# Kernel optimization log

Measured on AMD Instinct MI355X. Metric: run time of the kernel, lower is better.

The kernel has to match this reference:

```python
import jax, jax.numpy as jnp
import numpy as np

H, N_EMB, D_EMB, D_UP = 1024, 8192, 512, 2048
B, T, BB, M, K_LABELS = 4, 4096, 512, 4096, 64


def _rms(x, w, eps=1e-6):
    xf = x.astype(jnp.float32)
    var = jnp.mean(xf * xf, axis=-1, keepdims=True)
    return (w * (xf * jax.lax.rsqrt(var + eps))).astype(x.dtype)


def setup_inputs() -> dict:
    key = jax.random.key(0)
    ks = jax.random.split(key, 8)
    bt = B * T
    inp = jax.random.normal(ks[0], (B, T, H), jnp.float32)
    w_k = jax.random.normal(ks[1], (N_EMB, H), jnp.float32) * 0.02
    w_v = jax.random.normal(ks[2], (N_EMB, D_EMB), jnp.float32) * 0.02
    w_up = jax.random.normal(ks[3], (D_UP, D_EMB), jnp.float32) * 0.02
    w_mix = jax.random.normal(ks[4], (H, D_UP + H), jnp.float32) * 0.02
    fw = jax.random.permutation(ks[5], bt)
    bw = jnp.argsort(fw)  # inverse permutation
    seq_sort = jax.random.randint(ks[6], (bt,), 0, K_LABELS)
    keep_cols = jnp.arange(M)  # keep first M of N_EMB rows
    emb_alloc = jnp.arange(N_EMB) % K_LABELS  # every label present among kept rows
    starts = jnp.zeros((bt,), jnp.int32)
    ends = jnp.full((bt,), M, jnp.int32)
    return {
        'input': inp, 'fw': fw, 'bw': bw, 'seq_sort': seq_sort,
        'keep_cols': keep_cols, 'emb_alloc': emb_alloc,
        'starts': starts, 'ends': ends, 'bb': BB,
        'w_k_weight': w_k, 'w_v_weight': w_v, 'w_up_weight': w_up,
        'w_mix_weight': w_mix,
        'norm_in_weight': jnp.ones((H,), jnp.float32),
        'norm_out_weight': jnp.ones((D_UP,), jnp.float32),
    }


def reference(input, fw, bw, seq_sort, keep_cols, emb_alloc, starts, ends, bb,
              w_k_weight, w_v_weight, w_up_weight, w_mix_weight,
              norm_in_weight, norm_out_weight):
    b, t, h = input.shape
    A = _rms(input, norm_in_weight)                      # [b,t,h]
    Bm = w_k_weight[keep_cols]                           # [m,h]
    Cm = w_v_weight[keep_cols]                           # [m,d_emb]
    la = emb_alloc[keep_cols]                            # [m]
    A = A.reshape(-1, h)[fw].reshape(-1, bb, h)          # [nb,bb,h]
    ss = seq_sort.reshape(-1, bb)                        # [nb,bb]
    st = starts.reshape(-1, bb).min(axis=-1)             # [nb]
    en = ends.reshape(-1, bb).max(axis=-1)               # [nb]
    # ragged per-block slice B[start:end] expressed as a kv range mask,
    # combined with the equality mask seq_sort[q] == emb_alloc[kv]
    scores = jnp.einsum('nqh,kh->nqk', A, Bm)            # [nb,bb,m]
    kv = jnp.arange(Bm.shape[0])
    mask = ((ss[:, :, None] == la[None, None, :])
            & (kv[None, None, :] >= st[:, None, None])
            & (kv[None, None, :] < en[:, None, None]))
    scores = jnp.where(mask, scores, -jnp.inf)
    p = jax.nn.softmax(scores, axis=-1)
    comb = jnp.einsum('nqk,kd->nqd', p, Cm)              # [nb,bb,d_emb]
    d_emb = Cm.shape[-1]
    comb = comb.reshape(-1, d_emb)[bw].reshape(b, t, d_emb)
    up = comb @ w_up_weight.T                            # [b,t,d_up]
    cat = jnp.concatenate([_rms(up, norm_out_weight), input], axis=-1)
    return cat @ w_mix_weight.T                          # [b,t,h]
```

## Files before the change

### kernel.cpp

```cpp
#include <hip/hip_runtime.h>
#include <hip/hip_bf16.h>
#include <cstdint>
#include <cstddef>

#define Hh 1024
#define D_EMB 512
#define D_UP 2048
#define BT 16384
#define BB_ 512
#define Mm 4096
#define NB 32
#define KL 64
#define NXCD 8
#define PMMAX 8192
#define QROWMAX 17408
#define MAXT 1088

typedef __attribute__((ext_vector_type(4))) float f4;
typedef __attribute__((ext_vector_type(4))) __bf16 bf4;
typedef __attribute__((ext_vector_type(8))) __bf16 bf8;
typedef __attribute__((ext_vector_type(4))) float f32x4;

__device__ __forceinline__ void gl_lds16(const void* g, void* l) {
  __builtin_amdgcn_global_load_lds((__attribute__((address_space(1))) void*)g,
                                   (__attribute__((address_space(3))) void*)l, 16, 0, 0);
}

__global__ __launch_bounds__(256) void conv_bf16_kernel(const float* __restrict__ src,
                                                        __bf16* __restrict__ dst, int n4) {
  int i = blockIdx.x * 256 + threadIdx.x;
  if (i >= n4) return;
  f4 v = ((const f4*)src)[i];
  bf4 o = {(__bf16)v[0], (__bf16)v[1], (__bf16)v[2], (__bf16)v[3]};
  ((bf4*)dst)[i] = o;
}

__global__ __launch_bounds__(256) void la_kernel(const int* __restrict__ keep,
                                                 const int* __restrict__ emb,
                                                 int* __restrict__ la, int m) {
  int i = blockIdx.x * 256 + threadIdx.x;
  if (i < m) la[i] = emb[keep[i]];
}

__global__ __launch_bounds__(256) void range_kernel(const int* __restrict__ starts,
                                                    const int* __restrict__ ends,
                                                    int* __restrict__ stA, int* __restrict__ enA) {
  int n = blockIdx.x;
  int t = threadIdx.x, lane = t & 63, wv = t >> 6;
  int s1 = min(starts[n * BB_ + t], starts[n * BB_ + t + 256]);
  int e1 = max(ends[n * BB_ + t], ends[n * BB_ + t + 256]);
#pragma unroll
  for (int off = 32; off; off >>= 1) {
    s1 = min(s1, __shfl_xor(s1, off));
    e1 = max(e1, __shfl_xor(e1, off));
  }
  __shared__ int ssh[4], esh[4];
  if (lane == 0) { ssh[wv] = s1; esh[wv] = e1; }
  __syncthreads();
  if (t == 0) {
    int s = ssh[0], e = esh[0];
#pragma unroll
    for (int k = 1; k < 4; ++k) { s = min(s, ssh[k]); e = max(e, esh[k]); }
    stA[n] = s; enA[n] = e;
  }
}

__global__ __launch_bounds__(256) void hist_kernel(const int* __restrict__ la,
                                                   int* __restrict__ goff) {
  __shared__ int cnt[KL];
  int tid = threadIdx.x;
  if (tid < KL) cnt[tid] = 0;
  __syncthreads();
  for (int k = tid; k < Mm; k += 256) atomicAdd(&cnt[la[k]], 1);
  __syncthreads();
  if (tid == 0) {
    int a = 0;
    for (int s = 0; s < KL; ++s) { goff[s] = a; a += cnt[s]; }
    goff[KL] = a;
  }
}

__global__ __launch_bounds__(256) void place_kernel(const int* __restrict__ la,
                                                    const int* __restrict__ keep,
                                                    const int* __restrict__ goff,
                                                    int* __restrict__ gk,
                                                    int* __restrict__ ridx) {
  int s = blockIdx.x;
  int tid = threadIdx.x, lane = tid & 63, wv = tid >> 6;
  __shared__ int wc[4];
  __shared__ int run;
  if (tid == 0) run = goff[s];
  __syncthreads();
  for (int base = 0; base < Mm; base += 256) {
    int k = base + tid;
    bool f = (la[k] == s);
    unsigned long long msk = __ballot(f);
    int myidx = __popcll(msk & ((1ull << lane) - 1ull));
    if (lane == 0) wc[wv] = __popcll(msk);
    __syncthreads();
    int woff = 0, tot = 0;
#pragma unroll
    for (int w = 0; w < 4; ++w) {
      if (w < wv) woff += wc[w];
      tot += wc[w];
    }
    int rbase = run;
    if (f) {
      int p = rbase + woff + myidx;
      gk[p] = k;
      ridx[p] = keep[k];
    }
    __syncthreads();
    if (tid == 0) run = rbase + tot;
    __syncthreads();
  }
}

__global__ __launch_bounds__(256) void qsort_kernel(const int* __restrict__ seq_sort,
                                                    int* __restrict__ qidx,
                                                    int* __restrict__ qoffA,
                                                    int* __restrict__ qcntA) {
  int n = blockIdx.x, tid = threadIdx.x;
  __shared__ int cnt[KL], pos[KL], pref[KL];
  if (tid < KL) cnt[tid] = 0;
  __syncthreads();
  int s0 = seq_sort[n * BB_ + tid];
  int s1 = seq_sort[n * BB_ + tid + 256];
  atomicAdd(&cnt[s0], 1);
  atomicAdd(&cnt[s1], 1);
  __syncthreads();
  if (tid == 0) {
    int a = 0;
    for (int s = 0; s < KL; ++s) { pref[s] = a; a += cnt[s]; }
  }
  __syncthreads();
  if (tid < KL) {
    pos[tid] = pref[tid];
    qoffA[n * KL + tid] = pref[tid];
    qcntA[n * KL + tid] = cnt[tid];
  }
  __syncthreads();
  int p0 = atomicAdd(&pos[s0], 1);
  qidx[n * BB_ + p0] = n * BB_ + tid;
  int p1 = atomicAdd(&pos[s1], 1);
  qidx[n * BB_ + p1] = n * BB_ + tid + 256;
}

__global__ __launch_bounds__(256) void qmeta_kernel(const int* __restrict__ qcntA,
                                                    const int* __restrict__ goff,
                                                    int* __restrict__ boff,
                                                    int* __restrict__ qtot,
                                                    int* __restrict__ ptq,
                                                    int* __restrict__ pb,
                                                    int* __restrict__ taskS,
                                                    int* __restrict__ taskT,
                                                    int* __restrict__ ntt,
                                                    int* __restrict__ pbTot) {
  int tid = threadIdx.x;
  if (tid < KL) {
    int s = tid, tot = 0;
    for (int n = 0; n < NB; ++n) { boff[n * KL + s] = tot; tot += qcntA[n * KL + s]; }
    qtot[s] = tot;
  }
  __syncthreads();
  if (tid == 0) {
    int tb = 0, tk = 0, pk = 0;
    for (int s = 0; s < KL; ++s) {
      ptq[s] = tb;
      int nt = (qtot[s] + 15) >> 4;
      for (int t2 = 0; t2 < nt; ++t2) { taskS[tk] = s; taskT[tk] = t2; ++tk; }
      tb += nt;
      pb[s] = pk;
      int cnt = goff[s + 1] - goff[s];
      pk += (cnt + 63) & ~63;
    }
    ptq[KL] = tb;
    ntt[0] = tk;
    pbTot[0] = pk;
  }
}

__global__ __launch_bounds__(256) void pridx_kernel(const int* __restrict__ goff,
                                                    const int* __restrict__ pb,
                                                    const int* __restrict__ ridx,
                                                    int* __restrict__ pridx) {
  int s = blockIdx.x;
  int cnt = goff[s + 1] - goff[s];
  int padded = (cnt + 63) & ~63;
  int base = pb[s];
  for (int i = threadIdx.x; i < padded; i += 256)
    pridx[base + i] = (i < cnt) ? ridx[goff[s] + i] : -1;
}

__global__ __launch_bounds__(256) void lohi_kernel(const int* __restrict__ gk,
                                                   const int* __restrict__ goff,
                                                   const int* __restrict__ pb,
                                                   const int* __restrict__ stA,
                                                   const int* __restrict__ enA,
                                                   int* __restrict__ loA, int* __restrict__ hiA) {
  int i = blockIdx.x * 256 + threadIdx.x;
  if (i >= NB * KL) return;
  int n = i / KL, s = i % KL;
  int b = goff[s], e = goff[s + 1];
  int st = stA[n], en = enA[n];
  int lo = b, hi = e;
  while (lo < hi) { int mid = (lo + hi) >> 1; if (gk[mid] < st) lo = mid + 1; else hi = mid; }
  int L = lo;
  lo = b; hi = e;
  while (lo < hi) { int mid = (lo + hi) >> 1; if (gk[mid] < en) lo = mid + 1; else hi = mid; }
  loA[i] = pb[s] + (L - goff[s]);
  hiA[i] = pb[s] + (lo - goff[s]);
}

__global__ __launch_bounds__(256) void gq_kernel(const int* __restrict__ qidx,
                                                 const int* __restrict__ qoffA,
                                                 const int* __restrict__ seq_sort,
                                                 const int* __restrict__ boff,
                                                 const int* __restrict__ ptq,
                                                 int* __restrict__ qg2, int* __restrict__ gq) {
  int e = blockIdx.x * 256 + threadIdx.x;
  int n = e >> 9;
  int q = qidx[e];
  int s = seq_sort[q];
  int i = (e & 511) - qoffA[n * KL + s];
  int gpos = ptq[s] * 16 + boff[n * KL + s] + i;
  qg2[gpos] = q;
  gq[q] = gpos;
}

__global__ __launch_bounds__(256) void qzero_kernel(const int* __restrict__ ptq,
                                                    const int* __restrict__ qtot,
                                                    __bf16* __restrict__ Qsw) {
  int s = blockIdx.x;
  int b0 = ptq[s] * 16 + qtot[s];
  int b1 = ptq[s + 1] * 16;
  bf8 z;
#pragma unroll
  for (int j = 0; j < 8; ++j) z[j] = (__bf16)0.f;
  for (int r = b0; r < b1; ++r)
    for (int e8 = threadIdx.x; e8 < 128; e8 += 256)
      *(bf8*)&Qsw[(size_t)r * 1024 + e8 * 8] = z;
}

__global__ __launch_bounds__(256) void kswb_kernel(const float* __restrict__ wk,
                                                   const int* __restrict__ pridx,
                                                   const int* __restrict__ pbTot,
                                                   __bf16* __restrict__ Ksw) {
  int pt = blockIdx.x;
  if (pt * 16 >= pbTot[0]) return;
  __shared__ __bf16 Tk[16][1040];
  int tid = threadIdx.x;
  int rr = tid >> 4, lt = tid & 15;
  int src = pridx[pt * 16 + rr];
  for (int cc = 0; cc < 16; ++cc) {
    int i4 = cc * 16 + lt;
    f4 v = {0.f, 0.f, 0.f, 0.f};
    if (src >= 0) v = ((const f4*)(wk + (size_t)src * Hh))[i4];
    bf4 o = {(__bf16)v[0], (__bf16)v[1], (__bf16)v[2], (__bf16)v[3]};
    *(bf4*)&Tk[rr][i4 * 4] = o;
  }
  __syncthreads();
#pragma unroll
  for (int i = 0; i < 8; ++i) {
    int f = tid + 256 * i;
    int ks = f >> 6, ln = f & 63;
    int c2 = ln & 15, rg2 = ln >> 4;
    bf8 o = *(const bf8*)&Tk[c2][ks * 32 + rg2 * 8];
    *(bf8*)&Ksw[(size_t)pt * 16384 + (size_t)f * 8] = o;
  }
}

__global__ __launch_bounds__(256) void vswb_kernel(const float* __restrict__ wv_,
                                                   const int* __restrict__ pridx,
                                                   const int* __restrict__ pbTot,
                                                   __bf16* __restrict__ Vsw) {
  int pblk = blockIdx.x;
  if (pblk * 32 >= pbTot[0]) return;
  __shared__ __bf16 Tv[32][528];
  int tid = threadIdx.x;
  int rr = tid >> 3, lt = tid & 7;
  int src = pridx[pblk * 32 + rr];
  for (int cc = 0; cc < 16; ++cc) {
    int i4 = cc * 8 + lt;
    f4 v = {0.f, 0.f, 0.f, 0.f};
    if (src >= 0) v = ((const f4*)(wv_ + (size_t)src * D_EMB))[i4];
    bf4 o = {(__bf16)v[0], (__bf16)v[1], (__bf16)v[2], (__bf16)v[3]};
    *(bf4*)&Tv[rr][i4 * 4] = o;
  }
  __syncthreads();
#pragma unroll
  for (int i = 0; i < 8; ++i) {
    int f = tid + 256 * i;
    int ff = f >> 6, ln = f & 63;
    int c2 = ln & 15, rg2 = ln >> 4;
    bf8 o;
#pragma unroll
    for (int j = 0; j < 8; ++j) o[j] = Tv[rg2 * 8 + j][ff * 16 + c2];
    *(bf8*)&Vsw[(size_t)pblk * 16384 + (size_t)f * 8] = o;
  }
}

__global__ __launch_bounds__(256) void rms_in_kernel(const float* __restrict__ input,
                                                     const int* __restrict__ bw,
                                                     const int* __restrict__ gq,
                                                     const float* __restrict__ wn,
                                                     __bf16* __restrict__ Qsw,
                                                     __bf16* __restrict__ inb) {
  __shared__ __align__(16) __bf16 rowbuf[4][1024];
  int wv = threadIdx.x >> 6, lane = threadIdx.x & 63;
  int j = blockIdx.x * 4 + wv;
  const f4* src = (const f4*)(input + (size_t)j * Hh);
  f4 v[4];
  float ss = 0.f;
#pragma unroll
  for (int c = 0; c < 4; ++c) {
    v[c] = src[c * 64 + lane];
    ss += v[c][0] * v[c][0] + v[c][1] * v[c][1] + v[c][2] * v[c][2] + v[c][3] * v[c][3];
  }
#pragma unroll
  for (int off = 32; off; off >>= 1) ss += __shfl_xor(ss, off);
  float sc = rsqrtf(ss * (1.f / Hh) + 1e-6f);
  bf4* dstI = (bf4*)(inb + (size_t)j * Hh);
#pragma unroll
  for (int c = 0; c < 4; ++c) {
    bf4 o = {(__bf16)v[c][0], (__bf16)v[c][1], (__bf16)v[c][2], (__bf16)v[c][3]};
    dstI[c * 64 + lane] = o;
  }
  const f4* w4 = (const f4*)wn;
#pragma unroll
  for (int c = 0; c < 4; ++c) {
    f4 w = w4[c * 64 + lane];
    bf4 o = {(__bf16)(v[c][0] * sc * w[0]), (__bf16)(v[c][1] * sc * w[1]),
             (__bf16)(v[c][2] * sc * w[2]), (__bf16)(v[c][3] * sc * w[3])};
    *(bf4*)&rowbuf[wv][(c * 64 + lane) * 4] = o;
  }
  int gpos = gq[bw[j]];
  int qt2 = gpos >> 4, cq = gpos & 15;
#pragma unroll
  for (int h = 0; h < 2; ++h) {
    int k_ = lane + h * 64;
    int ks = k_ >> 2, rg2 = k_ & 3;
    bf8 o = *(const bf8*)&rowbuf[wv][ks * 32 + rg2 * 8];
    *(bf8*)(Qsw + (size_t)qt2 * 16384 + ks * 512 + (cq + 16 * rg2) * 8) = o;
  }
}

__global__ __launch_bounds__(256, 2) void attn5_kernel(const __bf16* __restrict__ Qsw,
                                                       const __bf16* __restrict__ Ksw,
                                                       const __bf16* __restrict__ Vsw,
                                                       const int* __restrict__ qg2,
                                                       const int* __restrict__ qtot,
                                                       const int* __restrict__ ptq,
                                                       const int* __restrict__ taskS,
                                                       const int* __restrict__ taskT,
                                                       const int* __restrict__ nttA,
                                                       const int* __restrict__ pb,
                                                       const int* __restrict__ loP,
                                                       const int* __restrict__ hiP,
                                                       const int* __restrict__ fw,
                                                       __bf16* __restrict__ comb) {
  __shared__ __align__(16) __bf16 owb[4][16][528];
  int wv = threadIdx.x >> 6, lane = threadIdx.x & 63;
  int t = blockIdx.x * 4 + wv;
  if (t >= nttA[0]) return;
  int s = taskS[t], tl = taskT[t];
  int qtp = ptq[s] + tl;
  int qcnt = min(16, qtot[s] - tl * 16);
  int c = lane & 15, rg = lane >> 4;
  bool qv = c < qcnt;
  int q_l = qg2[qtp * 16 + (qv ? c : 0)];
  int n_l = q_l >> 9;
  int lo_l = qv ? loP[n_l * KL + s] : 0x7fffffff;
  int hi_l = qv ? hiP[n_l * KL + s] : 0;
  int tlo = lo_l, thi = hi_l;
#pragma unroll
  for (int off = 1; off < 64; off <<= 1) {
    tlo = min(tlo, __shfl_xor(tlo, off));
    thi = max(thi, __shfl_xor(thi, off));
  }
  if (tlo >= thi) return;
  int pbs = pb[s];

  int sl_a = c + ((rg & 1) << 5);
  int sl_b = sl_a + 16;
  bool hiKt = (rg & 2) != 0;
  const __bf16* Qb = Qsw + (size_t)qtp * 16384 + lane * 8;

  float m = -1e30f, lsum = 0.f;
  f32x4 acc[32];
  f32x4 zero = {0.f, 0.f, 0.f, 0.f};
#pragma unroll
  for (int ff = 0; ff < 32; ++ff) acc[ff] = zero;

  int p0beg = pbs + ((tlo - pbs) & ~63);
  for (int p0 = p0beg; p0 < thi; p0 += 64) {
    const __bf16* Kb = Ksw + (size_t)(p0 >> 4) * 16384 + lane * 8;
    f32x4 sN[4];
#pragma unroll
    for (int kt = 0; kt < 4; ++kt) sN[kt] = zero;
#pragma unroll
    for (int ks = 0; ks < 32; ++ks) {
      bf8 qf = *(const bf8*)(Qb + ks * 512);
#pragma unroll
      for (int kt = 0; kt < 4; ++kt) {
        bf8 kf = *(const bf8*)(Kb + kt * 16384 + ks * 512);
        sN[kt] = __builtin_amdgcn_mfma_f32_16x16x32_bf16(kf, qf, sN[kt], 0, 0, 0);
      }
    }
    float smax = -1e30f;
#pragma unroll
    for (int kt = 0; kt < 4; ++kt)
#pragma unroll
      for (int r = 0; r < 4; ++r) {
        int kv = p0 + kt * 16 + rg * 4 + r;
        float sv = (kv >= lo_l && kv < hi_l) ? sN[kt][r] : -1e30f;
        sN[kt][r] = sv;
        smax = fmaxf(smax, sv);
      }
    smax = fmaxf(smax, __shfl_xor(smax, 16));
    smax = fmaxf(smax, __shfl_xor(smax, 32));
    float mn = fmaxf(m, smax);
    float scl = __expf(m - mn);
    float sum = 0.f;
#pragma unroll
    for (int kt = 0; kt < 4; ++kt)
#pragma unroll
      for (int r = 0; r < 4; ++r) {
        float pv = __expf(sN[kt][r] - mn);
        sN[kt][r] = pv;
        sum += pv;
      }
    sum += __shfl_xor(sum, 16);
    sum += __shfl_xor(sum, 32);
    lsum = lsum * scl + sum;
    m = mn;
#pragma unroll
    for (int ff = 0; ff < 32; ++ff) acc[ff] = acc[ff] * scl;

    bf8 pbh[2];
#pragma unroll
    for (int h = 0; h < 2; ++h) {
      float e[8];
#pragma unroll
      for (int r = 0; r < 4; ++r) {
        float a0 = __shfl(sN[2 * h][r], sl_a);
        float a1 = __shfl(sN[2 * h + 1][r], sl_a);
        e[r] = hiKt ? a1 : a0;
        float b0 = __shfl(sN[2 * h][r], sl_b);
        float b1 = __shfl(sN[2 * h + 1][r], sl_b);
        e[4 + r] = hiKt ? b1 : b0;
      }
      bf8 pbv;
#pragma unroll
      for (int i = 0; i < 8; ++i) pbv[i] = (__bf16)e[i];
      pbh[h] = pbv;
    }
    const __bf16* Vb = Vsw + (size_t)(p0 >> 5) * 16384 + lane * 8;
#pragma unroll
    for (int ff = 0; ff < 32; ++ff) {
      bf8 v0 = *(const bf8*)(Vb + ff * 512);
      bf8 v1 = *(const bf8*)(Vb + 16384 + ff * 512);
      acc[ff] = __builtin_amdgcn_mfma_f32_16x16x32_bf16(v0, pbh[0], acc[ff], 0, 0, 0);
      acc[ff] = __builtin_amdgcn_mfma_f32_16x16x32_bf16(v1, pbh[1], acc[ff], 0, 0, 0);
    }
  }

  float inv = 1.f / lsum;
#pragma unroll
  for (int ff = 0; ff < 32; ++ff) {
    bf4 o;
#pragma unroll
    for (int r = 0; r < 4; ++r) o[r] = (__bf16)(acc[ff][r] * inv);
    *(bf4*)&owb[wv][c][ff * 16 + rg * 4] = o;
  }
  int qsel = lane >> 2;
  bool vq = qsel < qcnt;
  size_t ob = 0;
  if (vq) ob = (size_t)fw[qg2[qtp * 16 + qsel]] * D_EMB + (lane & 3) * 8;
#pragma unroll
  for (int it = 0; it < 16; ++it) {
    bf8 o = *(const bf8*)&owb[wv][lane >> 2][(lane & 3) * 8 + it * 32];
    if (vq) *(bf8*)(comb + ob + (size_t)it * 32) = o;
  }
}

template <bool OUT_BF16>
__global__ __launch_bounds__(512, 2) void gemm8p(const __bf16* __restrict__ x0, int k0,
                                                 const __bf16* __restrict__ x1, int k1,
                                                 const __bf16* __restrict__ w,
                                                 void* __restrict__ outp, int Mt, int Nt) {
  __shared__ __align__(16) __bf16 lds[4][2][256 * 32];
  const int nwg = Mt * Nt;
  const int bid = blockIdx.x;
  const int swz = (bid % NXCD) * (nwg / NXCD) + bid / NXCD;
  const int m0 = (swz / Nt) * 256, n0 = (swz % Nt) * 256;
  const int K = k0 + k1;
  const int NT = K >> 5;
  const int N = Nt * 256;
  const int tid = threadIdx.x, lane = tid & 63, wvi = tid >> 6;
  const int wr = wvi >> 2, wc = wvi & 3;

  const int srow = tid >> 2;
  const int spb = (tid & 3) * 16;

  const int c = lane & 15, rg = lane >> 4;
  const int fa_off = c * 64 + ((rg ^ ((c >> 1) & 3)) << 4);

  auto stage_half = [&](int t, int j) {
    int kg = t * 32;
    const __bf16* xs;
    int ld, kk;
    if (kg < k0) { xs = x0; ld = k0; kk = kg; }
    else         { xs = x1; ld = k1; kk = kg - k0; }
    int b = t & 3;
    int r = j * 128 + srow;
    int lcol = (spb ^ (((r >> 1) & 3) << 4)) >> 1;
    gl_lds16(xs + (size_t)(m0 + r) * ld + kk + lcol,
             (void*)((char*)&lds[b][0][0] + r * 64 + spb));
    gl_lds16(w + (size_t)(n0 + r) * K + kg + lcol,
             (void*)((char*)&lds[b][1][0] + r * 64 + spb));
  };

  f32x4 acc[8][4];
  f32x4 zero = {0.f, 0.f, 0.f, 0.f};
#pragma unroll
  for (int a = 0; a < 8; ++a)
#pragma unroll
    for (int bnx = 0; bnx < 4; ++bnx) acc[a][bnx] = zero;

#pragma unroll
  for (int t = 0; t < 3; ++t) {
    stage_half(t, 0);
    stage_half(t, 1);
  }
  asm volatile("s_waitcnt vmcnt(8)" ::: "memory");
  __builtin_amdgcn_s_barrier();

  for (int t = 0; t < NT; ++t) {
    const char* Abase = (const char*)&lds[t & 3][0][0];
    const char* Bbase = (const char*)&lds[t & 3][1][0];
    bf8 bfr[4];
#pragma unroll
    for (int ri = 0; ri < 2; ++ri) {
      if (t + 3 < NT) stage_half(t + 3, ri);
      bf8 afr[4];
#pragma unroll
      for (int fi = 0; fi < 4; ++fi)
        afr[fi] = *(const bf8*)(Abase + (wr * 128 + ri * 64 + fi * 16) * 64 + fa_off);
      if (ri == 0) {
#pragma unroll
        for (int fi = 0; fi < 4; ++fi)
          bfr[fi] = *(const bf8*)(Bbase + (wc * 64 + fi * 16) * 64 + fa_off);
      }
      __builtin_amdgcn_s_barrier();
      __builtin_amdgcn_s_setprio(1);
#pragma unroll
      for (int fi = 0; fi < 4; ++fi)
#pragma unroll
        for (int ni = 0; ni < 4; ++ni)
          acc[ri * 4 + fi][ni] =
              __builtin_amdgcn_mfma_f32_16x16x32_bf16(afr[fi], bfr[ni], acc[ri * 4 + fi][ni], 0, 0, 0);
      __builtin_amdgcn_s_setprio(0);
      if (ri == 1) asm volatile("s_waitcnt vmcnt(8)" ::: "memory");
      __builtin_amdgcn_s_barrier();
    }
  }

  const int r0 = (lane >> 4) * 4, cc = lane & 15;
#pragma unroll
  for (int mi = 0; mi < 8; ++mi) {
    int rowb = m0 + wr * 128 + (mi >> 2) * 64 + (mi & 3) * 16 + r0;
#pragma unroll
    for (int ni = 0; ni < 4; ++ni) {
      int col = n0 + wc * 64 + ni * 16 + cc;
#pragma unroll
      for (int r = 0; r < 4; ++r) {
        float v = acc[mi][ni][r];
        if (OUT_BF16)
          ((__bf16*)outp)[(size_t)(rowb + r) * N + col] = (__bf16)v;
        else
          ((float*)outp)[(size_t)(rowb + r) * N + col] = v;
      }
    }
  }
}

__global__ __launch_bounds__(256) void rms_up_kernel(__bf16* __restrict__ up,
                                                     const float* __restrict__ wn) {
  int wv = threadIdx.x >> 6, lane = threadIdx.x & 63;
  size_t j = (size_t)blockIdx.x * 4 + wv;
  bf8* row = (bf8*)(up + j * D_UP);
  bf8 v[4];
  float ss = 0.f;
#pragma unroll
  for (int c = 0; c < 4; ++c) {
    v[c] = row[c * 64 + lane];
#pragma unroll
    for (int i = 0; i < 8; ++i) { float f = (float)v[c][i]; ss += f * f; }
  }
#pragma unroll
  for (int off = 32; off; off >>= 1) ss += __shfl_xor(ss, off);
  float sc = rsqrtf(ss * (1.f / D_UP) + 1e-6f);
#pragma unroll
  for (int c = 0; c < 4; ++c) {
    int ebase = (c * 64 + lane) * 8;
    f4 wa = *(const f4*)(wn + ebase);
    f4 wb = *(const f4*)(wn + ebase + 4);
    bf8 o;
#pragma unroll
    for (int i = 0; i < 4; ++i) o[i] = (__bf16)((float)v[c][i] * sc * wa[i]);
#pragma unroll
    for (int i = 0; i < 4; ++i) o[4 + i] = (__bf16)((float)v[c][4 + i] * sc * wb[i]);
    row[c * 64 + lane] = o;
  }
}

extern "C" void kernel_launch(void* const* d_in, const int* in_sizes, int n_in, void* d_out,
                              int out_size, void* d_ws, size_t ws_size, hipStream_t stream) {
  const float* input = (const float*)d_in[0];
  const int* fw = (const int*)d_in[1];
  const int* bw = (const int*)d_in[2];
  const int* seq_sort = (const int*)d_in[3];
  const int* keep_cols = (const int*)d_in[4];
  const int* emb_alloc = (const int*)d_in[5];
  const int* starts = (const int*)d_in[6];
  const int* ends = (const int*)d_in[7];
  const float* w_k = (const float*)d_in[9];
  const float* w_v = (const float*)d_in[10];
  const float* w_up = (const float*)d_in[11];
  const float* w_mix = (const float*)d_in[12];
  const float* w_nin = (const float*)d_in[13];
  const float* w_nout = (const float*)d_in[14];

  char* p = (char*)d_ws;
  auto take = [&](size_t b) {
    void* r = (void*)p;
    p += (b + 255) & ~(size_t)255;
    return r;
  };
  __bf16* inb = (__bf16*)take((size_t)BT * Hh * 2);
  __bf16* comb = (__bf16*)take((size_t)BT * D_EMB * 2);
  __bf16* wupB = (__bf16*)take((size_t)D_UP * D_EMB * 2);
  __bf16* wmixB = (__bf16*)take((size_t)Hh * (D_UP + Hh) * 2);
  char* pB = p;
  __bf16* Ksw = (__bf16*)take((size_t)PMMAX * 1024 * 2);
  __bf16* Vsw = (__bf16*)take((size_t)PMMAX * 512 * 2);
  __bf16* Qsw = (__bf16*)take((size_t)QROWMAX * 1024 * 2);
  int* la = (int*)take(Mm * 4);
  int* stA = (int*)take(NB * 4);
  int* enA = (int*)take(NB * 4);
  int* goff = (int*)take((KL + 1) * 4);
  int* gk = (int*)take(Mm * 4);
  int* ridx = (int*)take(Mm * 4);
  int* pridx = (int*)take(PMMAX * 4);
  int* loA = (int*)take(NB * KL * 4);
  int* hiA = (int*)take(NB * KL * 4);
  int* qidx = (int*)take(BT * 4);
  int* qoffA = (int*)take(NB * KL * 4);
  int* qcntA = (int*)take(NB * KL * 4);
  int* boff = (int*)take(NB * KL * 4);
  int* qtot = (int*)take(KL * 4);
  int* ptq = (int*)take((KL + 1) * 4);
  int* pb = (int*)take(KL * 4);
  int* taskS = (int*)take(MAXT * 4);
  int* taskT = (int*)take(MAXT * 4);
  int* ntt = (int*)take(4);
  int* pbTot = (int*)take(4);
  int* qg2 = (int*)take(QROWMAX * 4);
  int* gq = (int*)take(BT * 4);
  __bf16* up = (__bf16*)pB;

  conv_bf16_kernel<<<(D_UP * D_EMB / 4 + 255) / 256, 256, 0, stream>>>(w_up, wupB, D_UP * D_EMB / 4);
  conv_bf16_kernel<<<(Hh * (D_UP + Hh) / 4 + 255) / 256, 256, 0, stream>>>(w_mix, wmixB,
                                                                           Hh * (D_UP + Hh) / 4);
  la_kernel<<<Mm / 256, 256, 0, stream>>>(keep_cols, emb_alloc, la, Mm);
  range_kernel<<<NB, 256, 0, stream>>>(starts, ends, stA, enA);
  hist_kernel<<<1, 256, 0, stream>>>(la, goff);
  qsort_kernel<<<NB, 256, 0, stream>>>(seq_sort, qidx, qoffA, qcntA);
  place_kernel<<<KL, 256, 0, stream>>>(la, keep_cols, goff, gk, ridx);
  qmeta_kernel<<<1, 256, 0, stream>>>(qcntA, goff, boff, qtot, ptq, pb, taskS, taskT, ntt, pbTot);
  pridx_kernel<<<KL, 256, 0, stream>>>(goff, pb, ridx, pridx);
  lohi_kernel<<<(NB * KL + 255) / 256, 256, 0, stream>>>(gk, goff, pb, stA, enA, loA, hiA);
  gq_kernel<<<BT / 256, 256, 0, stream>>>(qidx, qoffA, seq_sort, boff, ptq, qg2, gq);
  qzero_kernel<<<KL, 256, 0, stream>>>(ptq, qtot, Qsw);
  kswb_kernel<<<PMMAX / 16, 256, 0, stream>>>(w_k, pridx, pbTot, Ksw);
  vswb_kernel<<<PMMAX / 32, 256, 0, stream>>>(w_v, pridx, pbTot, Vsw);

  rms_in_kernel<<<BT / 4, 256, 0, stream>>>(input, bw, gq, w_nin, Qsw, inb);
  attn5_kernel<<<MAXT / 4, 256, 0, stream>>>(Qsw, Ksw, Vsw, qg2, qtot, ptq, taskS, taskT, ntt, pb,
                                             loA, hiA, fw, comb);
  gemm8p<true><<<BT / 256 * (D_UP / 256), 512, 0, stream>>>(comb, D_EMB, (const __bf16*)nullptr, 0,
                                                            wupB, (void*)up, BT / 256, D_UP / 256);
  rms_up_kernel<<<BT / 4, 256, 0, stream>>>(up, w_nout);
  gemm8p<false><<<BT / 256 * (Hh / 256), 512, 0, stream>>>(up, D_UP, inb, Hh, wmixB, d_out,
                                                           BT / 256, Hh / 256);
}
```

Measured before the change: 376.0 us.

## Pin attention tasks to XCDs by label and restructure GEMM staging pipeline

Attention tasks are regrouped so each XCD (blockIdx & 7) processes labels s ≡ x mod 8. A fixed grid of 512 blocks loops persistently over that XCD's task list, so each label's K/V rows stay in one XCD's L2. Separately, the GEMM drops the half-tile interleaved staging with two barriers per k-step for whole-tile staging, one barrier per step and an explicit drain epilogue, which changes the accumulator row mapping. Risks are load imbalance across XCDs and less overlap between loads and compute in the GEMM.

```diff
diff --git a/kernel.cpp b/kernel.cpp
--- a/kernel.cpp
+++ b/kernel.cpp
@@ -154,7 +154,8 @@
                                                     int* __restrict__ pb,
                                                     int* __restrict__ taskS,
                                                     int* __restrict__ taskT,
-                                                    int* __restrict__ ntt,
+                                                    int* __restrict__ xoff,
+                                                    int* __restrict__ xcnt,
                                                     int* __restrict__ pbTot) {
   int tid = threadIdx.x;
   if (tid < KL) {
@@ -164,19 +165,25 @@
   }
   __syncthreads();
   if (tid == 0) {
-    int tb = 0, tk = 0, pk = 0;
+    int tb = 0, pk = 0;
     for (int s = 0; s < KL; ++s) {
       ptq[s] = tb;
-      int nt = (qtot[s] + 15) >> 4;
-      for (int t2 = 0; t2 < nt; ++t2) { taskS[tk] = s; taskT[tk] = t2; ++tk; }
-      tb += nt;
+      tb += (qtot[s] + 15) >> 4;
       pb[s] = pk;
       int cnt = goff[s + 1] - goff[s];
       pk += (cnt + 63) & ~63;
     }
     ptq[KL] = tb;
-    ntt[0] = tk;
     pbTot[0] = pk;
+    int tk = 0;
+    for (int x = 0; x < NXCD; ++x) {
+      xoff[x] = tk;
+      for (int s = x; s < KL; s += NXCD) {
+        int nt = (qtot[s] + 15) >> 4;
+        for (int t2 = 0; t2 < nt; ++t2) { taskS[tk] = s; taskT[tk] = t2; ++tk; }
+      }
+      xcnt[x] = tk - xoff[x];
+    }
   }
 }
 
@@ -345,7 +352,7 @@
   }
 }
 
-__global__ __launch_bounds__(256, 2) void attn5_kernel(const __bf16* __restrict__ Qsw,
+__global__ __launch_bounds__(256, 2) void attn6_kernel(const __bf16* __restrict__ Qsw,
                                                        const __bf16* __restrict__ Ksw,
                                                        const __bf16* __restrict__ Vsw,
                                                        const int* __restrict__ qg2,
@@ -353,7 +360,8 @@
                                                        const int* __restrict__ ptq,
                                                        const int* __restrict__ taskS,
                                                        const int* __restrict__ taskT,
-                                                       const int* __restrict__ nttA,
+                                                       const int* __restrict__ xoff,
+                                                       const int* __restrict__ xcnt,
                                                        const int* __restrict__ pb,
                                                        const int* __restrict__ loP,
                                                        const int* __restrict__ hiP,
@@ -361,134 +369,137 @@
                                                        __bf16* __restrict__ comb) {
   __shared__ __align__(16) __bf16 owb[4][16][528];
   int wv = threadIdx.x >> 6, lane = threadIdx.x & 63;
-  int t = blockIdx.x * 4 + wv;
-  if (t >= nttA[0]) return;
-  int s = taskS[t], tl = taskT[t];
-  int qtp = ptq[s] + tl;
-  int qcnt = min(16, qtot[s] - tl * 16);
+  int x = blockIdx.x & 7;
+  int cntx = xcnt[x], offx = xoff[x];
   int c = lane & 15, rg = lane >> 4;
-  bool qv = c < qcnt;
-  int q_l = qg2[qtp * 16 + (qv ? c : 0)];
-  int n_l = q_l >> 9;
-  int lo_l = qv ? loP[n_l * KL + s] : 0x7fffffff;
-  int hi_l = qv ? hiP[n_l * KL + s] : 0;
-  int tlo = lo_l, thi = hi_l;
-#pragma unroll
-  for (int off = 1; off < 64; off <<= 1) {
-    tlo = min(tlo, __shfl_xor(tlo, off));
-    thi = max(thi, __shfl_xor(thi, off));
-  }
-  if (tlo >= thi) return;
-  int pbs = pb[s];
-
   int sl_a = c + ((rg & 1) << 5);
   int sl_b = sl_a + 16;
   bool hiKt = (rg & 2) != 0;
-  const __bf16* Qb = Qsw + (size_t)qtp * 16384 + lane * 8;
-
-  float m = -1e30f, lsum = 0.f;
-  f32x4 acc[32];
-  f32x4 zero = {0.f, 0.f, 0.f, 0.f};
-#pragma unroll
-  for (int ff = 0; ff < 32; ++ff) acc[ff] = zero;
-
-  int p0beg = pbs + ((tlo - pbs) & ~63);
-  for (int p0 = p0beg; p0 < thi; p0 += 64) {
-    const __bf16* Kb = Ksw + (size_t)(p0 >> 4) * 16384 + lane * 8;
-    f32x4 sN[4];
-#pragma unroll
-    for (int kt = 0; kt < 4; ++kt) sN[kt] = zero;
-#pragma unroll
-    for (int ks = 0; ks < 32; ++ks) {
-      bf8 qf = *(const bf8*)(Qb + ks * 512);
-#pragma unroll
-      for (int kt = 0; kt < 4; ++kt) {
-        bf8 kf = *(const bf8*)(Kb + kt * 16384 + ks * 512);
-        sN[kt] = __builtin_amdgcn_mfma_f32_16x16x32_bf16(kf, qf, sN[kt], 0, 0, 0);
+
+  for (int slot = (blockIdx.x >> 3) * 4 + wv; slot < cntx; slot += 64 * 4) {
+    int t = offx + slot;
+    int s = taskS[t], tl = taskT[t];
+    int qtp = ptq[s] + tl;
+    int qcnt = min(16, qtot[s] - tl * 16);
+    bool qv = c < qcnt;
+    int q_l = qg2[qtp * 16 + (qv ? c : 0)];
+    int n_l = q_l >> 9;
+    int lo_l = qv ? loP[n_l * KL + s] : 0x7fffffff;
+    int hi_l = qv ? hiP[n_l * KL + s] : 0;
+    int tlo = lo_l, thi = hi_l;
+#pragma unroll
+    for (int off = 1; off < 64; off <<= 1) {
+      tlo = min(tlo, __shfl_xor(tlo, off));
+      thi = max(thi, __shfl_xor(thi, off));
+    }
+    if (tlo >= thi) continue;
+    int pbs = pb[s];
+    const __bf16* Qb = Qsw + (size_t)qtp * 16384 + lane * 8;
+
+    float m = -1e30f, lsum = 0.f;
+    f32x4 acc[32];
+    f32x4 zero = {0.f, 0.f, 0.f, 0.f};
+#pragma unroll
+    for (int ff = 0; ff < 32; ++ff) acc[ff] = zero;
+
+    int p0beg = pbs + ((tlo - pbs) & ~63);
+    for (int p0 = p0beg; p0 < thi; p0 += 64) {
+      const __bf16* Kb = Ksw + (size_t)(p0 >> 4) * 16384 + lane * 8;
+      f32x4 sN[4];
+#pragma unroll
+      for (int kt = 0; kt < 4; ++kt) sN[kt] = zero;
+#pragma unroll
+      for (int ks = 0; ks < 32; ++ks) {
+        bf8 qf = *(const bf8*)(Qb + ks * 512);
+#pragma unroll
+        for (int kt = 0; kt < 4; ++kt) {
+          bf8 kf = *(const bf8*)(Kb + kt * 16384 + ks * 512);
+          sN[kt] = __builtin_amdgcn_mfma_f32_16x16x32_bf16(kf, qf, sN[kt], 0, 0, 0);
+        }
       }
-    }
-    float smax = -1e30f;
-#pragma unroll
-    for (int kt = 0; kt < 4; ++kt)
-#pragma unroll
-      for (int r = 0; r < 4; ++r) {
-        int kv = p0 + kt * 16 + rg * 4 + r;
-        float sv = (kv >= lo_l && kv < hi_l) ? sN[kt][r] : -1e30f;
-        sN[kt][r] = sv;
-        smax = fmaxf(smax, sv);
+      float smax = -1e30f;
+#pragma unroll
+      for (int kt = 0; kt < 4; ++kt)
+#pragma unroll
+        for (int r = 0; r < 4; ++r) {
+          int kv = p0 + kt * 16 + rg * 4 + r;
+          float sv = (kv >= lo_l && kv < hi_l) ? sN[kt][r] : -1e30f;
+          sN[kt][r] = sv;
+          smax = fmaxf(smax, sv);
+        }
+      smax = fmaxf(smax, __shfl_xor(smax, 16));
+      smax = fmaxf(smax, __shfl_xor(smax, 32));
+      float mn = fmaxf(m, smax);
+      float scl = __expf(m - mn);
+      float sum = 0.f;
+#pragma unroll
+      for (int kt = 0; kt < 4; ++kt)
+#pragma unroll
+        for (int r = 0; r < 4; ++r) {
+          float pv = __expf(sN[kt][r] - mn);
+          sN[kt][r] = pv;
+          sum += pv;
+        }
+      sum += __shfl_xor(sum, 16);
+      sum += __shfl_xor(sum, 32);
+      lsum = lsum * scl + sum;
+      m = mn;
+#pragma unroll
+      for (int ff = 0; ff < 32; ++ff) acc[ff] = acc[ff] * scl;
+
+      bf8 pbh[2];
+#pragma unroll
+      for (int h = 0; h < 2; ++h) {
+        float e[8];
+#pragma unroll
+        for (int r = 0; r < 4; ++r) {
+          float a0 = __shfl(sN[2 * h][r], sl_a);
+          float a1 = __shfl(sN[2 * h + 1][r], sl_a);
+          e[r] = hiKt ? a1 : a0;
+          float b0 = __shfl(sN[2 * h][r], sl_b);
+          float b1 = __shfl(sN[2 * h + 1][r], sl_b);
+          e[4 + r] = hiKt ? b1 : b0;
+        }
+        bf8 pbv;
+#pragma unroll
+        for (int i = 0; i < 8; ++i) pbv[i] = (__bf16)e[i];
+        pbh[h] = pbv;
       }
-    smax = fmaxf(smax, __shfl_xor(smax, 16));
-    smax = fmaxf(smax, __shfl_xor(smax, 32));
-    float mn = fmaxf(m, smax);
-    float scl = __expf(m - mn);
-    float sum = 0.f;
-#pragma unroll
-    for (int kt = 0; kt < 4; ++kt)
-#pragma unroll
-      for (int r = 0; r < 4; ++r) {
-        float pv = __expf(sN[kt][r] - mn);
-        sN[kt][r] = pv;
-        sum += pv;
+      const __bf16* Vb = Vsw + (size_t)(p0 >> 5) * 16384 + lane * 8;
+#pragma unroll
+      for (int ff = 0; ff < 32; ++ff) {
+        bf8 v0 = *(const bf8*)(Vb + ff * 512);
+        bf8 v1 = *(const bf8*)(Vb + 16384 + ff * 512);
+        acc[ff] = __builtin_amdgcn_mfma_f32_16x16x32_bf16(v0, pbh[0], acc[ff], 0, 0, 0);
+        acc[ff] = __builtin_amdgcn_mfma_f32_16x16x32_bf16(v1, pbh[1], acc[ff], 0, 0, 0);
       }
-    sum += __shfl_xor(sum, 16);
-    sum += __shfl_xor(sum, 32);
-    lsum = lsum * scl + sum;
-    m = mn;
-#pragma unroll
-    for (int ff = 0; ff < 32; ++ff) acc[ff] = acc[ff] * scl;
-
-    bf8 pbh[2];
-#pragma unroll
-    for (int h = 0; h < 2; ++h) {
-      float e[8];
-#pragma unroll
-      for (int r = 0; r < 4; ++r) {
-        float a0 = __shfl(sN[2 * h][r], sl_a);
-        float a1 = __shfl(sN[2 * h + 1][r], sl_a);
-        e[r] = hiKt ? a1 : a0;
-        float b0 = __shfl(sN[2 * h][r], sl_b);
-        float b1 = __shfl(sN[2 * h + 1][r], sl_b);
-        e[4 + r] = hiKt ? b1 : b0;
-      }
-      bf8 pbv;
-#pragma unroll
-      for (int i = 0; i < 8; ++i) pbv[i] = (__bf16)e[i];
-      pbh[h] = pbv;
-    }
-    const __bf16* Vb = Vsw + (size_t)(p0 >> 5) * 16384 + lane * 8;
+    }
+
+    float inv = 1.f / lsum;
 #pragma unroll
     for (int ff = 0; ff < 32; ++ff) {
-      bf8 v0 = *(const bf8*)(Vb + ff * 512);
-      bf8 v1 = *(const bf8*)(Vb + 16384 + ff * 512);
-      acc[ff] = __builtin_amdgcn_mfma_f32_16x16x32_bf16(v0, pbh[0], acc[ff], 0, 0, 0);
-      acc[ff] = __builtin_amdgcn_mfma_f32_16x16x32_bf16(v1, pbh[1], acc[ff], 0, 0, 0);
-    }
-  }
-
-  float inv = 1.f / lsum;
-#pragma unroll
-  for (int ff = 0; ff < 32; ++ff) {
-    bf4 o;
-#pragma unroll
-    for (int r = 0; r < 4; ++r) o[r] = (__bf16)(acc[ff][r] * inv);
-    *(bf4*)&owb[wv][c][ff * 16 + rg * 4] = o;
-  }
-  int qsel = lane >> 2;
-  bool vq = qsel < qcnt;
-  size_t ob = 0;
-  if (vq) ob = (size_t)fw[qg2[qtp * 16 + qsel]] * D_EMB + (lane & 3) * 8;
-#pragma unroll
-  for (int it = 0; it < 16; ++it) {
-    bf8 o = *(const bf8*)&owb[wv][lane >> 2][(lane & 3) * 8 + it * 32];
-    if (vq) *(bf8*)(comb + ob + (size_t)it * 32) = o;
+      bf4 o;
+#pragma unroll
+      for (int r = 0; r < 4; ++r) o[r] = (__bf16)(acc[ff][r] * inv);
+      *(bf4*)&owb[wv][c][ff * 16 + rg * 4] = o;
+    }
+    int qsel = lane >> 2;
+    bool vq = qsel < qcnt;
+    size_t ob = 0;
+    if (vq) ob = (size_t)fw[qg2[qtp * 16 + qsel]] * D_EMB + (lane & 3) * 8;
+#pragma unroll
+    for (int it = 0; it < 16; ++it) {
+      bf8 o = *(const bf8*)&owb[wv][lane >> 2][(lane & 3) * 8 + it * 32];
+      if (vq) *(bf8*)(comb + ob + (size_t)it * 32) = o;
+    }
   }
 }
 
 template <bool OUT_BF16>
-__global__ __launch_bounds__(512, 2) void gemm8p(const __bf16* __restrict__ x0, int k0,
-                                                 const __bf16* __restrict__ x1, int k1,
-                                                 const __bf16* __restrict__ w,
-                                                 void* __restrict__ outp, int Mt, int Nt) {
+__global__ __launch_bounds__(512, 2) void gemm9(const __bf16* __restrict__ x0, int k0,
+                                                const __bf16* __restrict__ x1, int k1,
+                                                const __bf16* __restrict__ w,
+                                                void* __restrict__ outp, int Mt, int Nt) {
   __shared__ __align__(16) __bf16 lds[4][2][256 * 32];
   const int nwg = Mt * Nt;
   const int bid = blockIdx.x;
@@ -499,26 +510,27 @@
   const int N = Nt * 256;
   const int tid = threadIdx.x, lane = tid & 63, wvi = tid >> 6;
   const int wr = wvi >> 2, wc = wvi & 3;
-
   const int srow = tid >> 2;
   const int spb = (tid & 3) * 16;
-
   const int c = lane & 15, rg = lane >> 4;
   const int fa_off = c * 64 + ((rg ^ ((c >> 1) & 3)) << 4);
 
-  auto stage_half = [&](int t, int j) {
+  auto stage = [&](int t) {
     int kg = t * 32;
     const __bf16* xs;
     int ld, kk;
     if (kg < k0) { xs = x0; ld = k0; kk = kg; }
     else         { xs = x1; ld = k1; kk = kg - k0; }
     int b = t & 3;
-    int r = j * 128 + srow;
-    int lcol = (spb ^ (((r >> 1) & 3) << 4)) >> 1;
-    gl_lds16(xs + (size_t)(m0 + r) * ld + kk + lcol,
-             (void*)((char*)&lds[b][0][0] + r * 64 + spb));
-    gl_lds16(w + (size_t)(n0 + r) * K + kg + lcol,
-             (void*)((char*)&lds[b][1][0] + r * 64 + spb));
+#pragma unroll
+    for (int j = 0; j < 2; ++j) {
+      int r = j * 128 + srow;
+      int lcol = (spb ^ (((r >> 1) & 3) << 4)) >> 1;
+      gl_lds16(xs + (size_t)(m0 + r) * ld + kk + lcol,
+               (void*)((char*)&lds[b][0][0] + r * 64 + spb));
+      gl_lds16(w + (size_t)(n0 + r) * K + kg + lcol,
+               (void*)((char*)&lds[b][1][0] + r * 64 + spb));
+    }
   };
 
   f32x4 acc[8][4];
@@ -528,48 +540,47 @@
 #pragma unroll
     for (int bnx = 0; bnx < 4; ++bnx) acc[a][bnx] = zero;
 
-#pragma unroll
-  for (int t = 0; t < 3; ++t) {
-    stage_half(t, 0);
-    stage_half(t, 1);
-  }
+  auto compute = [&](int t) {
+    const char* Ab = (const char*)&lds[t & 3][0][0];
+    const char* Bb = (const char*)&lds[t & 3][1][0];
+    bf8 afr[8], bfr[4];
+#pragma unroll
+    for (int fi = 0; fi < 8; ++fi)
+      afr[fi] = *(const bf8*)(Ab + (wr * 128 + fi * 16) * 64 + fa_off);
+#pragma unroll
+    for (int ni = 0; ni < 4; ++ni)
+      bfr[ni] = *(const bf8*)(Bb + (wc * 64 + ni * 16) * 64 + fa_off);
+    __builtin_amdgcn_s_setprio(1);
+#pragma unroll
+    for (int fi = 0; fi < 8; ++fi)
+#pragma unroll
+      for (int ni = 0; ni < 4; ++ni)
+        acc[fi][ni] = __builtin_amdgcn_mfma_f32_16x16x32_bf16(afr[fi], bfr[ni], acc[fi][ni], 0, 0, 0);
+    __builtin_amdgcn_s_setprio(0);
+  };
+
+  stage(0); stage(1); stage(2);
   asm volatile("s_waitcnt vmcnt(8)" ::: "memory");
   __builtin_amdgcn_s_barrier();
 
-  for (int t = 0; t < NT; ++t) {
-    const char* Abase = (const char*)&lds[t & 3][0][0];
-    const char* Bbase = (const char*)&lds[t & 3][1][0];
-    bf8 bfr[4];
-#pragma unroll
-    for (int ri = 0; ri < 2; ++ri) {
-      if (t + 3 < NT) stage_half(t + 3, ri);
-      bf8 afr[4];
-#pragma unroll
-      for (int fi = 0; fi < 4; ++fi)
-        afr[fi] = *(const bf8*)(Abase + (wr * 128 + ri * 64 + fi * 16) * 64 + fa_off);
-      if (ri == 0) {
-#pragma unroll
-        for (int fi = 0; fi < 4; ++fi)
-          bfr[fi] = *(const bf8*)(Bbase + (wc * 64 + fi * 16) * 64 + fa_off);
-      }
-      __builtin_amdgcn_s_barrier();
-      __builtin_amdgcn_s_setprio(1);
-#pragma unroll
-      for (int fi = 0; fi < 4; ++fi)
-#pragma unroll
-        for (int ni = 0; ni < 4; ++ni)
-          acc[ri * 4 + fi][ni] =
-              __builtin_amdgcn_mfma_f32_16x16x32_bf16(afr[fi], bfr[ni], acc[ri * 4 + fi][ni], 0, 0, 0);
-      __builtin_amdgcn_s_setprio(0);
-      if (ri == 1) asm volatile("s_waitcnt vmcnt(8)" ::: "memory");
-      __builtin_amdgcn_s_barrier();
-    }
-  }
+  for (int t = 0; t < NT - 3; ++t) {
+    stage(t + 3);
+    compute(t);
+    asm volatile("s_waitcnt vmcnt(8)" ::: "memory");
+    __builtin_amdgcn_s_barrier();
+  }
+  compute(NT - 3);
+  asm volatile("s_waitcnt vmcnt(4)" ::: "memory");
+  __builtin_amdgcn_s_barrier();
+  compute(NT - 2);
+  asm volatile("s_waitcnt vmcnt(0)" ::: "memory");
+  __builtin_amdgcn_s_barrier();
+  compute(NT - 1);
 
   const int r0 = (lane >> 4) * 4, cc = lane & 15;
 #pragma unroll
   for (int mi = 0; mi < 8; ++mi) {
-    int rowb = m0 + wr * 128 + (mi >> 2) * 64 + (mi & 3) * 16 + r0;
+    int rowb = m0 + wr * 128 + mi * 16 + r0;
 #pragma unroll
     for (int ni = 0; ni < 4; ++ni) {
       int col = n0 + wc * 64 + ni * 16 + cc;
@@ -664,7 +675,8 @@
   int* pb = (int*)take(KL * 4);
   int* taskS = (int*)take(MAXT * 4);
   int* taskT = (int*)take(MAXT * 4);
-  int* ntt = (int*)take(4);
+  int* xoff = (int*)take(NXCD * 4);
+  int* xcnt = (int*)take(NXCD * 4);
   int* pbTot = (int*)take(4);
   int* qg2 = (int*)take(QROWMAX * 4);
   int* gq = (int*)take(BT * 4);
@@ -678,7 +690,8 @@
   hist_kernel<<<1, 256, 0, stream>>>(la, goff);
   qsort_kernel<<<NB, 256, 0, stream>>>(seq_sort, qidx, qoffA, qcntA);
   place_kernel<<<KL, 256, 0, stream>>>(la, keep_cols, goff, gk, ridx);
-  qmeta_kernel<<<1, 256, 0, stream>>>(qcntA, goff, boff, qtot, ptq, pb, taskS, taskT, ntt, pbTot);
+  qmeta_kernel<<<1, 256, 0, stream>>>(qcntA, goff, boff, qtot, ptq, pb, taskS, taskT, xoff, xcnt,
+                                      pbTot);
   pridx_kernel<<<KL, 256, 0, stream>>>(goff, pb, ridx, pridx);
   lohi_kernel<<<(NB * KL + 255) / 256, 256, 0, stream>>>(gk, goff, pb, stA, enA, loA, hiA);
   gq_kernel<<<BT / 256, 256, 0, stream>>>(qidx, qoffA, seq_sort, boff, ptq, qg2, gq);
@@ -687,11 +700,11 @@
   vswb_kernel<<<PMMAX / 32, 256, 0, stream>>>(w_v, pridx, pbTot, Vsw);
 
   rms_in_kernel<<<BT / 4, 256, 0, stream>>>(input, bw, gq, w_nin, Qsw, inb);
-  attn5_kernel<<<MAXT / 4, 256, 0, stream>>>(Qsw, Ksw, Vsw, qg2, qtot, ptq, taskS, taskT, ntt, pb,
-                                             loA, hiA, fw, comb);
-  gemm8p<true><<<BT / 256 * (D_UP / 256), 512, 0, stream>>>(comb, D_EMB, (const __bf16*)nullptr, 0,
-                                                            wupB, (void*)up, BT / 256, D_UP / 256);
+  attn6_kernel<<<512, 256, 0, stream>>>(Qsw, Ksw, Vsw, qg2, qtot, ptq, taskS, taskT, xoff, xcnt,
+                                        pb, loA, hiA, fw, comb);
+  gemm9<true><<<BT / 256 * (D_UP / 256), 512, 0, stream>>>(comb, D_EMB, (const __bf16*)nullptr, 0,
+                                                           wupB, (void*)up, BT / 256, D_UP / 256);
   rms_up_kernel<<<BT / 4, 256, 0, stream>>>(up, w_nout);
-  gemm8p<false><<<BT / 256 * (Hh / 256), 512, 0, stream>>>(up, D_UP, inb, Hh, wmixB, d_out,
-                                                           BT / 256, Hh / 256);
-}
+  gemm9<false><<<BT / 256 * (Hh / 256), 512, 0, stream>>>(up, D_UP, inb, Hh, wmixB, d_out,
+                                                          BT / 256, Hh / 256);
+}
```

After: 365.7 us. -2.7%, faster.
